# Optimization experiments

Hardware: AMD Instinct MI355X
Metric: run time of the kernel (lower is better)

## Reference

```python
import jax, jax.numpy as jnp
import numpy as np

B, T, C = 2, 2048, 2048
N_HEAD = 16

def setup_inputs() -> dict:
    key = jax.random.key(0)
    k1, k2, k3 = jax.random.split(key, 3)
    scale = 1.0 / np.sqrt(C)
    return {
        "x": jax.random.normal(k1, (B, T, C), dtype=jnp.float32),
        "w_attn": jax.random.normal(k2, (C, 3 * C), dtype=jnp.float32) * scale,
        "b_attn": jnp.zeros((3 * C,), dtype=jnp.float32),
        "w_proj": jax.random.normal(k3, (C, C), dtype=jnp.float32) * scale,
        "b_proj": jnp.zeros((C,), dtype=jnp.float32),
    }

def reference(x, w_attn, b_attn, w_proj, b_proj):
    Bb, Tt, Cc = x.shape
    hd = Cc // N_HEAD  # head_size
    qkv = x @ w_attn + b_attn              # [B,T,3C]
    q, k, v = jnp.split(qkv, 3, axis=-1)
    # [B,T,C] -> [B,H,T,hd]
    def heads(t):
        return t.reshape(Bb, Tt, N_HEAD, hd).transpose(0, 2, 1, 3)
    q, k, v = heads(q), heads(k), heads(v)
    att = jnp.einsum("bhqd,bhkd->bhqk", q, k) * (hd ** -0.5)
    causal = jnp.tril(jnp.ones((Tt, Tt), dtype=bool))
    att = jnp.where(causal[None, None], att, -jnp.inf)
    att = jax.nn.softmax(att, axis=-1)
    out = jnp.einsum("bhqk,bhkd->bhqd", att, v)
    out = out.transpose(0, 2, 1, 3).reshape(Bb, Tt, Cc)
    return out @ w_proj + b_proj
```

## Files before the change

### kernel.cpp

```cpp
#include <hip/hip_runtime.h>
#include <cstdint>
#include <cstddef>

typedef __bf16 bf16_t;
typedef __bf16 bf16x8 __attribute__((ext_vector_type(8)));
typedef __bf16 bf16x4 __attribute__((ext_vector_type(4)));
typedef float floatx4 __attribute__((ext_vector_type(4)));

#define B_  2
#define T_  2048
#define C_  2048
#define H_  16
#define HD_ 128

#define K_ATTN_SCALE (0.08838834764831843f * 1.44269504088896f)

__device__ __forceinline__ void async_copy16(const void* g, void* l) {
  __builtin_amdgcn_global_load_lds((const __attribute__((address_space(1))) unsigned int*)g,
                                   (__attribute__((address_space(3))) unsigned int*)l,
                                   16, 0, 0);
}

__global__ __launch_bounds__(256) void cvt_f32_bf16(const float* __restrict__ in,
                                                    bf16_t* __restrict__ out, int n4) {
  int i = blockIdx.x * 256 + threadIdx.x;
  if (i >= n4) return;
  const float4 v = ((const float4*)in)[i];
  bf16x4 o;
  o[0] = (bf16_t)v.x; o[1] = (bf16_t)v.y; o[2] = (bf16_t)v.z; o[3] = (bf16_t)v.w;
  ((bf16x4*)out)[i] = o;
}

__global__ __launch_bounds__(256) void transpose_cvt(const float* __restrict__ W,
                                                     bf16_t* __restrict__ Wt,
                                                     int Kd, int Nd) {
  __shared__ float tile[32][33];
  const int tx = threadIdx.x, ty = threadIdx.y;
  const int n0 = blockIdx.x * 32, k0 = blockIdx.y * 32;
#pragma unroll
  for (int j = ty; j < 32; j += 8)
    tile[j][tx] = W[(size_t)(k0 + j) * Nd + n0 + tx];
  __syncthreads();
#pragma unroll
  for (int j = ty; j < 32; j += 8)
    Wt[(size_t)(n0 + j) * Kd + k0 + tx] = (bf16_t)tile[tx][j];
}

#define GBM 256
#define GBN 256
#define GBK 64

__global__ __launch_bounds__(512, 2) void gemm_qkv(
    const bf16_t* __restrict__ A, const bf16_t* __restrict__ Bt,
    const float* __restrict__ bias,
    bf16_t* __restrict__ Qo, bf16_t* __restrict__ Ko, bf16_t* __restrict__ Vo,
    int K) {
  __shared__ __align__(16) char smem[131072];
  const int tid = threadIdx.x;
  const int wave = tid >> 6, lane = tid & 63;
  const int quad = lane >> 4, l15 = lane & 15;
  const int wm = wave >> 2, wn = wave & 3;
  const int bm = blockIdx.y * GBM, bn = blockIdx.x * GBN;

  const bf16_t* asrc[4];
  const bf16_t* bsrc[4];
#pragma unroll
  for (int l = 0; l < 4; ++l) {
    int p = l * 8192 + tid * 16;
    int r = p >> 7;
    int c = (p & 127) ^ ((r & 7) << 4);
    asrc[l] = A  + (size_t)(bm + r) * K + (c >> 1);
    bsrc[l] = Bt + (size_t)(bn + r) * K + (c >> 1);
  }

  auto stage = [&](int buf, int k0) {
    char* As = smem + buf * 65536;
    char* Bs = As + 32768;
#pragma unroll
    for (int l = 0; l < 4; ++l) {
      int p = l * 8192 + tid * 16;
      async_copy16(asrc[l] + k0, As + p);
      async_copy16(bsrc[l] + k0, Bs + p);
    }
  };

  const int sx = (l15 & 7) << 4;
  const int cq = quad * 16;
  const int arow = (wm * 128 + l15) << 7;
  const int brow = (wn * 64 + l15) << 7;

  floatx4 acc[8][4] = {};

  stage(0, 0);
  asm volatile("s_waitcnt vmcnt(0)" ::: "memory");
  __builtin_amdgcn_s_barrier();

  const int NT = K / GBK;
  for (int t = 0; t < NT; ++t) {
    const int buf = t & 1;
    const char* As = smem + buf * 65536;
    const char* Bs = As + 32768;
    if (t + 1 < NT) stage(buf ^ 1, (t + 1) * GBK);

#pragma unroll
    for (int mq = 0; mq < 2; ++mq) {
      bf16x8 af[4][2];
#pragma unroll
      for (int i = 0; i < 4; ++i)
#pragma unroll
        for (int ks = 0; ks < 2; ++ks)
          af[i][ks] = *(const bf16x8*)(As + arow + (((mq * 64 + i * 16)) << 7) +
                                       ((ks * 64 + cq) ^ sx));
#pragma unroll
      for (int nq = 0; nq < 2; ++nq) {
        bf16x8 bfr[2][2];
#pragma unroll
        for (int j = 0; j < 2; ++j)
#pragma unroll
          for (int ks = 0; ks < 2; ++ks)
            bfr[j][ks] = *(const bf16x8*)(Bs + brow + (((nq * 32 + j * 16)) << 7) +
                                          ((ks * 64 + cq) ^ sx));
        __builtin_amdgcn_s_barrier();
        __builtin_amdgcn_s_setprio(1);
#pragma unroll
        for (int i = 0; i < 4; ++i)
#pragma unroll
          for (int j = 0; j < 2; ++j)
#pragma unroll
            for (int ks = 0; ks < 2; ++ks)
              acc[mq * 4 + i][nq * 2 + j] = __builtin_amdgcn_mfma_f32_16x16x32_bf16(
                  af[i][ks], bfr[j][ks], acc[mq * 4 + i][nq * 2 + j], 0, 0, 0);
        __builtin_amdgcn_s_setprio(0);
        if (mq == 1 && nq == 1)
          asm volatile("s_waitcnt vmcnt(0)" ::: "memory");
        __builtin_amdgcn_s_barrier();
      }
    }
  }

  float bias_r[4];
#pragma unroll
  for (int jj = 0; jj < 4; ++jj)
    bias_r[jj] = bias[bn + wn * 64 + (jj >> 1) * 32 + (jj & 1) * 16 + l15];

  if (bn < 2 * C_) {
    const int which = bn >> 11;
    bf16_t* dst0 = which ? Ko : Qo;
    const float scl = which ? 1.0f : K_ATTN_SCALE;
#pragma unroll
    for (int ii = 0; ii < 8; ++ii) {
      const int m = bm + wm * 128 + (ii >> 2) * 64 + (ii & 3) * 16 + quad * 4;
      const int b = m >> 11, tq = m & 2047;
#pragma unroll
      for (int jj = 0; jj < 4; ++jj) {
        const int n = bn + wn * 64 + (jj >> 1) * 32 + (jj & 1) * 16 + l15;
        const int cc = n & 2047;
        const int h = cc >> 7, d = cc & 127;
        bf16_t* dst = dst0 + (((size_t)(b * H_ + h)) * T_ + tq) * HD_ + d;
#pragma unroll
        for (int r = 0; r < 4; ++r)
          dst[(size_t)r * HD_] = (bf16_t)((acc[ii][jj][r] + bias_r[jj]) * scl);
      }
    }
  } else {
    __syncthreads();
    bf16_t* vt = (bf16_t*)smem;
#pragma unroll
    for (int ii = 0; ii < 8; ++ii) {
      const int tl = wm * 128 + (ii >> 2) * 64 + (ii & 3) * 16 + quad * 4;
#pragma unroll
      for (int jj = 0; jj < 4; ++jj) {
        const int dl = wn * 64 + (jj >> 1) * 32 + (jj & 1) * 16 + l15;
        const int sw = 8 * (dl & 15);
#pragma unroll
        for (int r = 0; r < 4; ++r)
          vt[dl * 256 + ((tl + r) ^ sw)] = (bf16_t)(acc[ii][jj][r] + bias_r[jj]);
      }
    }
    __syncthreads();
    const int dr = tid >> 1, half = tid & 1;
    const int h = ((bn - 2 * C_) >> 7) + (dr >> 7);
    const int b = bm >> 11, t0g = bm & 2047;
    bf16_t* dst = Vo + ((size_t)(b * H_ + h) * HD_ + (dr & 127)) * T_ + t0g;
#pragma unroll
    for (int cc2 = 0; cc2 < 16; ++cc2) {
      const int c = half * 16 + cc2;
      uint4 v = *(const uint4*)&vt[dr * 256 + ((c ^ (dr & 15)) * 8)];
      *(uint4*)(dst + c * 8) = v;
    }
  }
}

#define TM 128
#define TN 128
#define BK 64

__global__ __launch_bounds__(256) void gemm_proj(
    const bf16_t* __restrict__ A, const bf16_t* __restrict__ Bt,
    const float* __restrict__ bias, float* __restrict__ Cout,
    int M, int N, int K) {
  __shared__ __align__(16) char smem[32768];
  bf16_t (*As)[BK] = (bf16_t(*)[BK])smem;
  bf16_t (*Bs)[BK] = (bf16_t(*)[BK])(smem + 16384);
  const int tid = threadIdx.x;
  const int wave = tid >> 6, lane = tid & 63;
  const int quad = lane >> 4, l15 = lane & 15;
  const int bm = blockIdx.y * TM, bn = blockIdx.x * TN;
  const int wm = (wave >> 1) * 64, wn = (wave & 1) * 64;
  const int sw = l15 & 7;

  floatx4 acc[4][4] = {};

  for (int k0 = 0; k0 < K; k0 += BK) {
#pragma unroll
    for (int it = 0; it < 4; ++it) {
      int p = it * 4096 + tid * 16;
      int r = p >> 7;
      int cg = ((p >> 4) & 7) ^ (r & 7);
      async_copy16(A + (size_t)(bm + r) * K + k0 + cg * 8, (char*)&As[0][0] + p);
      async_copy16(Bt + (size_t)(bn + r) * K + k0 + cg * 8, (char*)&Bs[0][0] + p);
    }
    __syncthreads();
#pragma unroll
    for (int kc = 0; kc < 2; ++kc) {
      const int cidx = (kc * 4 + quad) ^ sw;
      bf16x8 af[4], bf[4];
#pragma unroll
      for (int i = 0; i < 4; ++i)
        af[i] = *(const bf16x8*)&As[wm + i * 16 + l15][cidx * 8];
#pragma unroll
      for (int j = 0; j < 4; ++j)
        bf[j] = *(const bf16x8*)&Bs[wn + j * 16 + l15][cidx * 8];
#pragma unroll
      for (int i = 0; i < 4; ++i)
#pragma unroll
        for (int j = 0; j < 4; ++j)
          acc[i][j] = __builtin_amdgcn_mfma_f32_16x16x32_bf16(af[i], bf[j], acc[i][j], 0, 0, 0);
    }
    __syncthreads();
  }

#pragma unroll
  for (int i = 0; i < 4; ++i) {
#pragma unroll
    for (int j = 0; j < 4; ++j) {
#pragma unroll
      for (int r = 0; r < 4; ++r) {
        int m = bm + wm + i * 16 + quad * 4 + r;
        int n = bn + wn + j * 16 + l15;
        Cout[(size_t)m * N + n] = acc[i][j][r] + bias[n];
      }
    }
  }
}

__global__ __launch_bounds__(256) void attn(const bf16_t* __restrict__ Q,
                                            const bf16_t* __restrict__ Kg,
                                            const bf16_t* __restrict__ Vt,
                                            bf16_t* __restrict__ O) {
  __shared__ bf16_t Ks[2][64][128];
  __shared__ bf16_t Vs[2][128][64];
  const int tid = threadIdx.x;
  const int wave = tid >> 6, lane = tid & 63;
  const int quad = lane >> 4, l15 = lane & 15;
  const int j = blockIdx.x;
  const int bh = blockIdx.y;
  const int b = bh >> 4, h = bh & 15;
  const int qtA = 31 - j, qtB = j;
  const int nchA = qtA + 1, nchB = qtB + 1;
  const int q0A = qtA * 64 + wave * 16;
  const int q0B = qtB * 64 + wave * 16;

  const bf16_t* Qh = Q + (size_t)bh * T_ * HD_;
  const bf16_t* Kh = Kg + (size_t)bh * T_ * HD_;
  const bf16_t* Vh = Vt + (size_t)bh * HD_ * T_;

  bf16x8 qfA[4], qfB[4];
#pragma unroll
  for (int kk = 0; kk < 4; ++kk) {
    qfA[kk] = *(const bf16x8*)(Qh + (size_t)(q0A + l15) * HD_ + kk * 32 + quad * 8);
    qfB[kk] = *(const bf16x8*)(Qh + (size_t)(q0B + l15) * HD_ + kk * 32 + quad * 8);
  }

  floatx4 oaccA[8] = {}, oaccB[8] = {};
  float l_A = 0.0f, l_B = 0.0f;

  union PU { bf16x4 v; long long u; };
  union PF { long long u[2]; bf16x8 v; };
  const int lo = ((lane & 16) << 1) + l15;

  auto stage = [&](int buf, int kt0) {
#pragma unroll
    for (int it = 0; it < 4; ++it) {
      int p = it * 4096 + tid * 16;
      int r = p >> 8;
      int cg = ((p >> 4) & 15) ^ (r & 15);
      async_copy16(Kh + (size_t)(kt0 + r) * HD_ + cg * 8, (char*)&Ks[buf][0][0] + p);
    }
#pragma unroll
    for (int it = 0; it < 4; ++it) {
      int p = it * 4096 + tid * 16;
      int r = p >> 7;
      int cg = ((p >> 4) & 7) ^ (r & 7);
      async_copy16(Vh + (size_t)r * T_ + kt0 + cg * 8, (char*)&Vs[buf][0][0] + p);
    }
  };

  auto step = [&](int buf, const bf16x8* qf, floatx4* oacc, float& l_i, int q0, int kt0,
                  bool mask) {
    floatx4 s[4] = {{}, {}, {}, {}};
#pragma unroll
    for (int st = 0; st < 4; ++st) {
#pragma unroll
      for (int kk = 0; kk < 4; ++kk) {
        bf16x8 kf = *(const bf16x8*)&Ks[buf][st * 16 + l15][(((kk * 4 + quad) ^ l15) & 15) * 8];
        s[st] = __builtin_amdgcn_mfma_f32_16x16x32_bf16(kf, qf[kk], s[st], 0, 0, 0);
      }
    }
    float ps = 0.0f;
    long long pu[4];
#pragma unroll
    for (int st = 0; st < 4; ++st) {
      PU t;
#pragma unroll
      for (int r = 0; r < 4; ++r) {
        float val = s[st][r];
        if (mask) {
          int kt = kt0 + st * 16 + quad * 4 + r;
          val = (kt <= q0 + l15) ? val : -3.0e38f;
        }
        float p = exp2f(val);
        ps += p;
        t.v[r] = (bf16_t)p;
      }
      pu[st] = t.u;
    }
    ps += __shfl_xor(ps, 16);
    ps += __shfl_xor(ps, 32);
    l_i += ps;
#pragma unroll
    for (int bb = 0; bb < 2; ++bb) {
      long long lo0 = __shfl(pu[2 * bb], lo);
      long long hi0 = __shfl(pu[2 * bb], lo + 16);
      long long lo1 = __shfl(pu[2 * bb + 1], lo);
      long long hi1 = __shfl(pu[2 * bb + 1], lo + 16);
      PF pf;
      pf.u[0] = (quad >= 2) ? lo1 : lo0;
      pf.u[1] = (quad >= 2) ? hi1 : hi0;
#pragma unroll
      for (int dt = 0; dt < 8; ++dt) {
        bf16x8 vf = *(const bf16x8*)&Vs[buf][dt * 16 + l15][(((bb * 4 + quad) ^ l15) & 7) * 8];
        oacc[dt] = __builtin_amdgcn_mfma_f32_16x16x32_bf16(pf.v, vf, oacc[dt], 0, 0, 0);
      }
    }
  };

  stage(0, 0);
  for (int ch = 0; ch < nchA; ++ch) {
    __syncthreads();
    if (ch + 1 < nchA) stage((ch + 1) & 1, (ch + 1) * 64);
    const int kt0 = ch * 64;
    const int buf = ch & 1;
    step(buf, qfA, oaccA, l_A, q0A, kt0, ch == nchA - 1);
    if (ch < nchB) step(buf, qfB, oaccB, l_B, q0B, kt0, ch == nchB - 1);
  }

  float lrA[4], lrB[4];
#pragma unroll
  for (int r = 0; r < 4; ++r) {
    lrA[r] = __shfl(l_A, quad * 4 + r);
    lrB[r] = __shfl(l_B, quad * 4 + r);
  }
#pragma unroll
  for (int dt = 0; dt < 8; ++dt) {
#pragma unroll
    for (int r = 0; r < 4; ++r) {
      int d = dt * 16 + l15;
      int qa = q0A + quad * 4 + r;
      int qb = q0B + quad * 4 + r;
      O[((size_t)(b * T_ + qa)) * C_ + h * HD_ + d] = (bf16_t)(oaccA[dt][r] / lrA[r]);
      O[((size_t)(b * T_ + qb)) * C_ + h * HD_ + d] = (bf16_t)(oaccB[dt][r] / lrB[r]);
    }
  }
}

extern "C" void kernel_launch(void* const* d_in, const int* in_sizes, int n_in,
                              void* d_out, int out_size, void* d_ws, size_t ws_size,
                              hipStream_t stream) {
  const float* x      = (const float*)d_in[0];
  const float* w_attn = (const float*)d_in[1];
  const float* b_attn = (const float*)d_in[2];
  const float* w_proj = (const float*)d_in[3];
  const float* b_proj = (const float*)d_in[4];
  float* out = (float*)d_out;

  char* p = (char*)d_ws;
  bf16_t* xb  = (bf16_t*)p; p += (size_t)4096 * 2048 * 2;
  bf16_t* waT = (bf16_t*)p; p += (size_t)6144 * 2048 * 2;
  bf16_t* wpT = (bf16_t*)p; p += (size_t)2048 * 2048 * 2;
  bf16_t* Qb  = (bf16_t*)p; p += (size_t)32 * 2048 * 128 * 2;
  bf16_t* Kb  = (bf16_t*)p; p += (size_t)32 * 2048 * 128 * 2;
  bf16_t* Vb  = (bf16_t*)p; p += (size_t)32 * 2048 * 128 * 2;
  bf16_t* Ob  = (bf16_t*)p; p += (size_t)4096 * 2048 * 2;

  cvt_f32_bf16<<<8192, 256, 0, stream>>>(x, xb, 2097152);
  transpose_cvt<<<dim3(6144 / 32, 2048 / 32), dim3(32, 8), 0, stream>>>(w_attn, waT, 2048, 6144);
  transpose_cvt<<<dim3(2048 / 32, 2048 / 32), dim3(32, 8), 0, stream>>>(w_proj, wpT, 2048, 2048);

  gemm_qkv<<<dim3(6144 / GBN, 4096 / GBM), 512, 0, stream>>>(
      xb, waT, b_attn, Qb, Kb, Vb, 2048);

  attn<<<dim3(16, 32), 256, 0, stream>>>(Qb, Kb, Vb, Ob);

  gemm_proj<<<dim3(2048 / TN, 4096 / TM), 256, 0, stream>>>(
      Ob, wpT, b_proj, out, 4096, 2048, 2048);
}
```

Baseline: 429.7 us.

## Triple-buffer QKV GEMM with K=32 tiles and split A/B staged loads

Rewrites the QKV GEMM main loop to use BK=32 with three LDS buffers and a two-tile-ahead prefetch. A and B global-to-LDS loads are issued separately, each interleaved with one half of the MFMA work, and vmcnt waits are relaxed to keep loads in flight. The LDS swizzle and fragment layout change to fit the 64-byte rows. The intent is to hide global load latency better. The cost is more barriers per unit of K work and per-tile overhead from the smaller K step.

Result: no change. 434.4 us (+1.1%).

```diff
diff --git a/kernel.cpp b/kernel.cpp
--- a/kernel.cpp
+++ b/kernel.cpp
@@ -48,7 +48,7 @@
 
 #define GBM 256
 #define GBN 256
-#define GBK 64
+#define GBK 32
 
 __global__ __launch_bounds__(512, 2) void gemm_qkv(
     const bf16_t* __restrict__ A, const bf16_t* __restrict__ Bt,
@@ -62,119 +62,135 @@
   const int wm = wave >> 2, wn = wave & 3;
   const int bm = blockIdx.y * GBM, bn = blockIdx.x * GBN;
 
-  const bf16_t* asrc[4];
-  const bf16_t* bsrc[4];
-#pragma unroll
-  for (int l = 0; l < 4; ++l) {
+  const bf16_t* asrc[2];
+  const bf16_t* bsrc[2];
+#pragma unroll
+  for (int l = 0; l < 2; ++l) {
     int p = l * 8192 + tid * 16;
-    int r = p >> 7;
-    int c = (p & 127) ^ ((r & 7) << 4);
-    asrc[l] = A  + (size_t)(bm + r) * K + (c >> 1);
-    bsrc[l] = Bt + (size_t)(bn + r) * K + (c >> 1);
-  }
-
-  auto stage = [&](int buf, int k0) {
-    char* As = smem + buf * 65536;
-    char* Bs = As + 32768;
-#pragma unroll
-    for (int l = 0; l < 4; ++l) {
-      int p = l * 8192 + tid * 16;
-      async_copy16(asrc[l] + k0, As + p);
-      async_copy16(bsrc[l] + k0, Bs + p);
-    }
+    int r = p >> 6;
+    int c = ((p >> 4) & 3) ^ (r & 3);
+    asrc[l] = A  + (size_t)(bm + r) * K + c * 8;
+    bsrc[l] = Bt + (size_t)(bn + r) * K + c * 8;
+  }
+
+  auto stageA = [&](int buf, int k0) {
+    char* As = smem + buf * 32768;
+#pragma unroll
+    for (int l = 0; l < 2; ++l)
+      async_copy16(asrc[l] + k0, As + l * 8192 + tid * 16);
   };
-
-  const int sx = (l15 & 7) << 4;
+  auto stageB = [&](int buf, int k0) {
+    char* Bs = smem + buf * 32768 + 16384;
+#pragma unroll
+    for (int l = 0; l < 2; ++l)
+      async_copy16(bsrc[l] + k0, Bs + l * 8192 + tid * 16);
+  };
+
+  const int sx = (l15 & 3) << 4;
   const int cq = quad * 16;
-  const int arow = (wm * 128 + l15) << 7;
-  const int brow = (wn * 64 + l15) << 7;
+  const int arow = (wm * 128 + l15) * 64;
+  const int brow = (wn * 64 + l15) * 64;
 
   floatx4 acc[8][4] = {};
-
-  stage(0, 0);
-  asm volatile("s_waitcnt vmcnt(0)" ::: "memory");
+  bf16x8 af[8], bfr[4];
+
+  stageA(0, 0); stageB(0, 0);
+  stageA(1, GBK); stageB(1, GBK);
+  asm volatile("s_waitcnt vmcnt(4)" ::: "memory");
   __builtin_amdgcn_s_barrier();
 
   const int NT = K / GBK;
+  int cur = 0;
   for (int t = 0; t < NT; ++t) {
-    const int buf = t & 1;
-    const char* As = smem + buf * 65536;
-    const char* Bs = As + 32768;
-    if (t + 1 < NT) stage(buf ^ 1, (t + 1) * GBK);
-
-#pragma unroll
-    for (int mq = 0; mq < 2; ++mq) {
-      bf16x8 af[4][2];
-#pragma unroll
-      for (int i = 0; i < 4; ++i)
-#pragma unroll
-        for (int ks = 0; ks < 2; ++ks)
-          af[i][ks] = *(const bf16x8*)(As + arow + (((mq * 64 + i * 16)) << 7) +
-                                       ((ks * 64 + cq) ^ sx));
-#pragma unroll
-      for (int nq = 0; nq < 2; ++nq) {
-        bf16x8 bfr[2][2];
-#pragma unroll
-        for (int j = 0; j < 2; ++j)
-#pragma unroll
-          for (int ks = 0; ks < 2; ++ks)
-            bfr[j][ks] = *(const bf16x8*)(Bs + brow + (((nq * 32 + j * 16)) << 7) +
-                                          ((ks * 64 + cq) ^ sx));
-        __builtin_amdgcn_s_barrier();
-        __builtin_amdgcn_s_setprio(1);
-#pragma unroll
-        for (int i = 0; i < 4; ++i)
-#pragma unroll
-          for (int j = 0; j < 2; ++j)
-#pragma unroll
-            for (int ks = 0; ks < 2; ++ks)
-              acc[mq * 4 + i][nq * 2 + j] = __builtin_amdgcn_mfma_f32_16x16x32_bf16(
-                  af[i][ks], bfr[j][ks], acc[mq * 4 + i][nq * 2 + j], 0, 0, 0);
-        __builtin_amdgcn_s_setprio(0);
-        if (mq == 1 && nq == 1)
-          asm volatile("s_waitcnt vmcnt(0)" ::: "memory");
-        __builtin_amdgcn_s_barrier();
-      }
-    }
+    const char* As = smem + cur * 32768;
+    const char* Bs = As + 16384;
+    int nxt = cur + 2; if (nxt >= 3) nxt -= 3;
+    const bool st = (t + 2 < NT);
+
+#pragma unroll
+    for (int j = 0; j < 4; ++j)
+      bfr[j] = *(const bf16x8*)(Bs + brow + j * 16 * 64 + (cq ^ sx));
+#pragma unroll
+    for (int i = 0; i < 4; ++i)
+      af[i] = *(const bf16x8*)(As + arow + i * 16 * 64 + (cq ^ sx));
+    if (st) stageA(nxt, (t + 2) * GBK);
+    __builtin_amdgcn_sched_barrier(0);
+    __builtin_amdgcn_s_barrier();
+    asm volatile("s_waitcnt lgkmcnt(0)" ::: "memory");
+    __builtin_amdgcn_sched_barrier(0);
+    __builtin_amdgcn_s_setprio(1);
+#pragma unroll
+    for (int i = 0; i < 4; ++i)
+#pragma unroll
+      for (int j = 0; j < 4; ++j)
+        acc[i][j] = __builtin_amdgcn_mfma_f32_16x16x32_bf16(af[i], bfr[j], acc[i][j], 0, 0, 0);
+    __builtin_amdgcn_s_setprio(0);
+    __builtin_amdgcn_sched_barrier(0);
+    __builtin_amdgcn_s_barrier();
+
+#pragma unroll
+    for (int i = 4; i < 8; ++i)
+      af[i] = *(const bf16x8*)(As + arow + i * 16 * 64 + (cq ^ sx));
+    if (st) stageB(nxt, (t + 2) * GBK);
+    __builtin_amdgcn_sched_barrier(0);
+    __builtin_amdgcn_s_barrier();
+    asm volatile("s_waitcnt lgkmcnt(0)" ::: "memory");
+    __builtin_amdgcn_sched_barrier(0);
+    __builtin_amdgcn_s_setprio(1);
+#pragma unroll
+    for (int i = 4; i < 8; ++i)
+#pragma unroll
+      for (int j = 0; j < 4; ++j)
+        acc[i][j] = __builtin_amdgcn_mfma_f32_16x16x32_bf16(af[i], bfr[j], acc[i][j], 0, 0, 0);
+    __builtin_amdgcn_s_setprio(0);
+    __builtin_amdgcn_sched_barrier(0);
+
+    if (t < NT - 2) {
+      asm volatile("s_waitcnt vmcnt(4)" ::: "memory");
+    } else if (t == NT - 2) {
+      asm volatile("s_waitcnt vmcnt(0)" ::: "memory");
+    }
+    __builtin_amdgcn_s_barrier();
+    cur = cur + 1; if (cur >= 3) cur -= 3;
   }
 
   float bias_r[4];
 #pragma unroll
-  for (int jj = 0; jj < 4; ++jj)
-    bias_r[jj] = bias[bn + wn * 64 + (jj >> 1) * 32 + (jj & 1) * 16 + l15];
+  for (int j = 0; j < 4; ++j)
+    bias_r[j] = bias[bn + wn * 64 + j * 16 + l15];
 
   if (bn < 2 * C_) {
     const int which = bn >> 11;
     bf16_t* dst0 = which ? Ko : Qo;
     const float scl = which ? 1.0f : K_ATTN_SCALE;
 #pragma unroll
-    for (int ii = 0; ii < 8; ++ii) {
-      const int m = bm + wm * 128 + (ii >> 2) * 64 + (ii & 3) * 16 + quad * 4;
+    for (int i = 0; i < 8; ++i) {
+      const int m = bm + wm * 128 + i * 16 + quad * 4;
       const int b = m >> 11, tq = m & 2047;
 #pragma unroll
-      for (int jj = 0; jj < 4; ++jj) {
-        const int n = bn + wn * 64 + (jj >> 1) * 32 + (jj & 1) * 16 + l15;
+      for (int j = 0; j < 4; ++j) {
+        const int n = bn + wn * 64 + j * 16 + l15;
         const int cc = n & 2047;
         const int h = cc >> 7, d = cc & 127;
         bf16_t* dst = dst0 + (((size_t)(b * H_ + h)) * T_ + tq) * HD_ + d;
 #pragma unroll
         for (int r = 0; r < 4; ++r)
-          dst[(size_t)r * HD_] = (bf16_t)((acc[ii][jj][r] + bias_r[jj]) * scl);
+          dst[(size_t)r * HD_] = (bf16_t)((acc[i][j][r] + bias_r[j]) * scl);
       }
     }
   } else {
     __syncthreads();
     bf16_t* vt = (bf16_t*)smem;
 #pragma unroll
-    for (int ii = 0; ii < 8; ++ii) {
-      const int tl = wm * 128 + (ii >> 2) * 64 + (ii & 3) * 16 + quad * 4;
-#pragma unroll
-      for (int jj = 0; jj < 4; ++jj) {
-        const int dl = wn * 64 + (jj >> 1) * 32 + (jj & 1) * 16 + l15;
+    for (int i = 0; i < 8; ++i) {
+      const int tl = wm * 128 + i * 16 + quad * 4;
+#pragma unroll
+      for (int j = 0; j < 4; ++j) {
+        const int dl = wn * 64 + j * 16 + l15;
         const int sw = 8 * (dl & 15);
 #pragma unroll
         for (int r = 0; r < 4; ++r)
-          vt[dl * 256 + ((tl + r) ^ sw)] = (bf16_t)(acc[ii][jj][r] + bias_r[jj]);
+          vt[dl * 256 + ((tl + r) ^ sw)] = (bf16_t)(acc[i][j][r] + bias_r[j]);
       }
     }
     __syncthreads();
```
